# Performance work log

Measured on AMD Instinct MI355X. Metric: run time of the kernel, lower is better.

The kernel has to match this reference:

```python
import jax, jax.numpy as jnp
import numpy as np

TABLE = 4194304   # maxGridFeatId[-1]
D = 4             # eachGridFeatDim
L = 6             # gridFeatLevelCnt (code indexes sigma1..sigma6)
DIR = 16          # in_dim_dir
H = 64            # hidden_dim_color
B, N = 16384, 128


def _linear_init(key, fan_in, fan_out):
    # matches torch nn.Linear default U(-1/sqrt(fan_in), 1/sqrt(fan_in))
    s = 1.0 / np.sqrt(fan_in)
    kw, kb = jax.random.split(key)
    W = jax.random.uniform(kw, (fan_in, fan_out), minval=-s, maxval=s, dtype=jnp.float32)
    b = jax.random.uniform(kb, (fan_out,), minval=-s, maxval=s, dtype=jnp.float32)
    return W, b


def setup_inputs() -> dict:
    key = jax.random.key(0)
    ks = jax.random.split(key, 6)
    x = jax.random.randint(ks[0], (B, N, L), 0, TABLE)
    d = jax.random.normal(ks[1], (B, DIR), dtype=jnp.float32)
    gridWeight = jax.random.uniform(ks[2], (TABLE, D), dtype=jnp.float32)  # torch.rand
    in0 = DIR + L * (D - 1)  # 16 + 18 = 34
    W0, b0 = _linear_init(ks[3], in0, H)
    W1, b1 = _linear_init(ks[4], H, H)
    W2, b2 = _linear_init(ks[5], H, 3)
    return dict(x=x, d=d, gridWeight=gridWeight, W0=W0, b0=b0, W1=W1, b1=b1, W2=W2, b2=b2)


def reference(x, d, gridWeight, W0, b0, W1, b1, W2, b2):
    Bv, Nv, Lv = x.shape
    Dv = gridWeight.shape[-1]
    # embedding gather: (B, N, L, D); same memory order as torch reshape(B, N*L, D)
    feat = gridWeight[x]
    # per-level densities, clipped then multiplied (prod over the 6 levels)
    sig = jnp.clip(feat[..., 0], 0.0, 1.0)                 # (B, N, L)
    sigma0 = jnp.prod(sig, axis=-1, keepdims=True) + 1e-4  # (B, N, 1)
    sigma = sigma0 / jnp.max(sigma0, axis=1, keepdims=True)
    # geometric features: (B, N, L*(D-1))
    geo = feat[..., 1:].reshape(Bv, Nv, Lv * (Dv - 1))
    h = jnp.concatenate([jnp.broadcast_to(d[:, None, :], (Bv, Nv, d.shape[-1])), geo], axis=-1)
    h = jax.nn.relu(h @ W0 + b0)
    h = jax.nn.relu(h @ W1 + b1)
    color = jax.nn.sigmoid(h @ W2 + b2)                    # (B, N, 3)
    # alpha compositing: NOTE original does torch.cumprod(..., dim=2) on a
    # (B, N, 1) tensor, i.e. cumprod over a size-1 axis == identity. Faithful.
    alpha = 1.0 - sigma
    transparentBefore = jnp.concatenate(
        [jnp.ones((Bv, 1, 1), dtype=sigma.dtype), alpha[:, :-1]], axis=1)
    colorWeight0 = transparentBefore * sigma               # (B, N, 1)
    colorOut = colorWeight0 * color                        # (B, N, 3)
    return sigma, jnp.sum(colorOut, axis=1)                # (B,N,1), (B,3)
```

## Files before the change

### kernel.cpp

```cpp
#include <hip/hip_runtime.h>
#include <math.h>


typedef short bf16x8 __attribute__((ext_vector_type(8)));
typedef float floatx4 __attribute__((ext_vector_type(4)));

__device__ inline unsigned short f2b(float f) {
    union { float f; unsigned u; } v; v.f = f;
    unsigned r = v.u + 0x7FFF + ((v.u >> 16) & 1);
    return (unsigned short)(r >> 16);
}

__global__ void build_frags(const float* __restrict__ W0,
                            const float* __restrict__ W1,
                            const float* __restrict__ W2,
                            unsigned short* __restrict__ wsf) {
    int tid = blockIdx.x * blockDim.x + threadIdx.x;
    if (tid >= 7168) return;
    int lane, j, k, n;
    float val;
    if (tid < 2048) {
        int f = tid >> 9, r = tid & 511; lane = r >> 3; j = r & 7;
        k = ((lane >> 4) * 8) + j;
        n = f * 16 + (lane & 15);
        val = (k < 18) ? W0[(16 + k) * 64 + n] : 0.0f;
    } else if (tid < 6144) {
        int e = tid - 2048;
        int f = e >> 9, r = e & 511; lane = r >> 3; j = r & 7;
        int ks = f >> 2, nt = f & 3;
        k = ks * 32 + ((lane >> 4) * 8) + j;
        n = nt * 16 + (lane & 15);
        val = W1[k * 64 + n];
    } else {
        int e = tid - 6144;
        int f = e >> 9, r = e & 511; lane = r >> 3; j = r & 7;
        k = f * 32 + ((lane >> 4) * 8) + j;
        n = lane & 15;
        val = (n < 3) ? W2[k * 3 + n] : 0.0f;
    }
    wsf[tid] = f2b(val);
}

__global__ __launch_bounds__(512, 4) void surf_main(
    const int*   __restrict__ x,
    const float* __restrict__ dvec,
    const float* __restrict__ gw,
    const float* __restrict__ W0,
    const float* __restrict__ b0,
    const float* __restrict__ b1,
    const float* __restrict__ b2,
    const unsigned short* __restrict__ wsf,
    float* __restrict__ out_sigma,
    float* __restrict__ out_color)
{
    const int b    = blockIdx.x;
    const int t    = threadIdx.x;
    const int lane = t & 63;
    const int w    = t >> 6;
    const int l15  = lane & 15;
    const int quad = lane >> 4;

    __shared__ unsigned short A0[128 * 40];
    __shared__ unsigned short H1[128 * 72];
    __shared__ float s_sigl[768];
    __shared__ float s_dirW[64];
    __shared__ float s_wmax[2];
    __shared__ float s_cw[128];
    __shared__ float s_part[8 * 16];

    bf16x8 bw0[4], bw1[8];
    #pragma unroll
    for (int i = 0; i < 4; ++i) bw0[i] = *(const bf16x8*)(wsf + i * 512 + lane * 8);
    #pragma unroll
    for (int i = 0; i < 8; ++i) bw1[i] = *(const bf16x8*)(wsf + 2048 + i * 512 + lane * 8);

    #pragma unroll
    for (int e0 = 0; e0 < 768; e0 += 512) {
        int e = e0 + t;
        if (e < 768) {
            int xv = x[(size_t)b * 768 + e];
            int point = e / 6;
            int level = e - point * 6;
            float4 v = *(const float4*)(gw + (size_t)xv * 4);
            s_sigl[e] = fminf(fmaxf(v.x, 0.0f), 1.0f);
            unsigned short* a = A0 + point * 40 + level * 3;
            a[0] = f2b(v.y); a[1] = f2b(v.z); a[2] = f2b(v.w);
        }
    }
    if (t < 128) {
        unsigned short* a = A0 + t * 40;
        *(unsigned int*)(a + 18) = 0u;
        *(uint2*)(a + 20) = make_uint2(0u, 0u);
        *(uint2*)(a + 24) = make_uint2(0u, 0u);
        *(uint2*)(a + 28) = make_uint2(0u, 0u);
    }
    if (t < 64) {
        float acc = b0[t];
        const float* db = dvec + (size_t)b * 16;
        #pragma unroll
        for (int i = 0; i < 16; ++i) acc = fmaf(db[i], W0[i * 64 + t], acc);
        s_dirW[t] = acc;
    }
    __syncthreads();

    float sigma0 = 0.0f;
    if (t < 128) {
        float p = 1.0f;
        #pragma unroll
        for (int l = 0; l < 6; ++l) p *= s_sigl[t * 6 + l];
        sigma0 = p + 1e-4f;
        float m = sigma0;
        #pragma unroll
        for (int off = 32; off; off >>= 1) m = fmaxf(m, __shfl_xor(m, off));
        if (lane == 0) s_wmax[w] = m;
    }
    __syncthreads();
    if (t < 128) {
        float maxv  = fmaxf(s_wmax[0], s_wmax[1]);
        float sigma = sigma0 / maxv;
        out_sigma[(size_t)b * 128 + t] = sigma;
        float cw;
        if (t == 0) cw = sigma;
        else {
            float pp = 1.0f;
            #pragma unroll
            for (int l = 0; l < 6; ++l) pp *= s_sigl[(t - 1) * 6 + l];
            float sprev = (pp + 1e-4f) / maxv;
            cw = (1.0f - sprev) * sigma;
        }
        s_cw[t] = cw;
    }

    const int row = w * 16 + l15;
    bf16x8 a0 = *(const bf16x8*)(A0 + row * 40 + quad * 8);
    floatx4 acc0[4];
    #pragma unroll
    for (int nt = 0; nt < 4; ++nt) {
        float dw = s_dirW[nt * 16 + l15];
        acc0[nt] = (floatx4){dw, dw, dw, dw};
        acc0[nt] = __builtin_amdgcn_mfma_f32_16x16x32_bf16(a0, bw0[nt], acc0[nt], 0, 0, 0);
    }
    #pragma unroll
    for (int nt = 0; nt < 4; ++nt)
        #pragma unroll
        for (int r = 0; r < 4; ++r) {
            int pr = w * 16 + quad * 4 + r;
            H1[pr * 72 + nt * 16 + l15] = f2b(fmaxf(acc0[nt][r], 0.0f));
        }

    bf16x8 a1a = *(const bf16x8*)(H1 + row * 72 + quad * 8);
    bf16x8 a1b = *(const bf16x8*)(H1 + row * 72 + 32 + quad * 8);
    floatx4 acc1[4];
    #pragma unroll
    for (int nt = 0; nt < 4; ++nt) {
        float bb = b1[nt * 16 + l15];
        acc1[nt] = (floatx4){bb, bb, bb, bb};
        acc1[nt] = __builtin_amdgcn_mfma_f32_16x16x32_bf16(a1a, bw1[nt],     acc1[nt], 0, 0, 0);
        acc1[nt] = __builtin_amdgcn_mfma_f32_16x16x32_bf16(a1b, bw1[4 + nt], acc1[nt], 0, 0, 0);
    }
    #pragma unroll
    for (int nt = 0; nt < 4; ++nt)
        #pragma unroll
        for (int r = 0; r < 4; ++r) {
            int pr = w * 16 + quad * 4 + r;
            H1[pr * 72 + nt * 16 + l15] = f2b(fmaxf(acc1[nt][r], 0.0f));
        }

    bf16x8 bw2a = *(const bf16x8*)(wsf + 6144 + lane * 8);
    bf16x8 bw2b = *(const bf16x8*)(wsf + 6144 + 512 + lane * 8);
    bf16x8 a2a = *(const bf16x8*)(H1 + row * 72 + quad * 8);
    bf16x8 a2b = *(const bf16x8*)(H1 + row * 72 + 32 + quad * 8);
    float bias2 = (l15 < 3) ? b2[l15] : 0.0f;
    floatx4 acc2 = (floatx4){bias2, bias2, bias2, bias2};
    acc2 = __builtin_amdgcn_mfma_f32_16x16x32_bf16(a2a, bw2a, acc2, 0, 0, 0);
    acc2 = __builtin_amdgcn_mfma_f32_16x16x32_bf16(a2b, bw2b, acc2, 0, 0, 0);

    __syncthreads();
    float sum = 0.0f;
    #pragma unroll
    for (int r = 0; r < 4; ++r) {
        float col = 1.0f / (1.0f + __expf(-acc2[r]));
        float cw  = s_cw[w * 16 + quad * 4 + r];
        sum += cw * col;
    }
    sum += __shfl_xor(sum, 16);
    sum += __shfl_xor(sum, 32);
    if (lane < 16) s_part[w * 16 + lane] = sum;
    __syncthreads();
    if (t < 3) {
        float o = 0.0f;
        #pragma unroll
        for (int ww = 0; ww < 8; ++ww) o += s_part[ww * 16 + t];
        out_color[(size_t)b * 3 + t] = o;
    }
}

extern "C" void kernel_launch(void* const* d_in, const int* in_sizes, int n_in,
                              void* d_out, int out_size, void* d_ws, size_t ws_size,
                              hipStream_t stream) {
    const int*   x    = (const int*)d_in[0];
    const float* dvec = (const float*)d_in[1];
    const float* gw   = (const float*)d_in[2];
    const float* W0   = (const float*)d_in[3];
    const float* b0   = (const float*)d_in[4];
    const float* W1   = (const float*)d_in[5];
    const float* b1   = (const float*)d_in[6];
    const float* W2   = (const float*)d_in[7];
    const float* b2   = (const float*)d_in[8];

    const int B = in_sizes[1] / 16;
    float* out_sigma = (float*)d_out;
    float* out_color = (float*)d_out + (size_t)B * 128;
    unsigned short* wsf = (unsigned short*)d_ws;

    build_frags<<<14, 512, 0, stream>>>(W0, W1, W2, wsf);
    surf_main<<<B, 512, 0, stream>>>(x, dvec, gw, W0, b0, b1, b2, wsf,
                                     out_sigma, out_color);
}
```

Baseline: 338.3 us.

## Hoist gather loads, pack bf16 conversions, swizzle A0 layout, raise occupancy

Issues the x index and grid-feature gathers at kernel entry, before the weight-fragment loads, so the random global reads start earlier. Rewrites the A0 tile as a 32-column XOR-swizzled layout, with each level stored as a padded 4-element packed write, and remaps the W0 fragments to match. Replaces the software bf16 rounding with the hardware v_cvt_pk_bf16_f32 instruction and raises the launch-bounds occupancy hint from 4 to 8. The higher occupancy hint may force register spills, since each thread holds 12 weight fragments plus the early-loaded feature values.

```diff
diff --git a/kernel.cpp b/kernel.cpp
--- a/kernel.cpp
+++ b/kernel.cpp
@@ -4,11 +4,18 @@
 
 typedef short bf16x8 __attribute__((ext_vector_type(8)));
 typedef float floatx4 __attribute__((ext_vector_type(4)));
+typedef float f32x4  __attribute__((ext_vector_type(4)));
 
 __device__ inline unsigned short f2b(float f) {
     union { float f; unsigned u; } v; v.f = f;
     unsigned r = v.u + 0x7FFF + ((v.u >> 16) & 1);
     return (unsigned short)(r >> 16);
+}
+
+__device__ inline unsigned cvt_pk_bf16(float a, float b) {
+    unsigned r;
+    asm("v_cvt_pk_bf16_f32 %0, %1, %2" : "=v"(r) : "v"(a), "v"(b));
+    return r;
 }
 
 __global__ void build_frags(const float* __restrict__ W0,
@@ -21,9 +28,10 @@
     float val;
     if (tid < 2048) {
         int f = tid >> 9, r = tid & 511; lane = r >> 3; j = r & 7;
-        k = ((lane >> 4) * 8) + j;
+        int kp  = ((lane >> 4) * 8) + j;
+        int lev = kp >> 2, c = kp & 3;
         n = f * 16 + (lane & 15);
-        val = (k < 18) ? W0[(16 + k) * 64 + n] : 0.0f;
+        val = (lev < 6 && c < 3) ? W0[(16 + lev * 3 + c) * 64 + n] : 0.0f;
     } else if (tid < 6144) {
         int e = tid - 2048;
         int f = e >> 9, r = e & 511; lane = r >> 3; j = r & 7;
@@ -41,7 +49,7 @@
     wsf[tid] = f2b(val);
 }
 
-__global__ __launch_bounds__(512, 4) void surf_main(
+__global__ __launch_bounds__(512, 8) void surf_main(
     const int*   __restrict__ x,
     const float* __restrict__ dvec,
     const float* __restrict__ gw,
@@ -60,7 +68,7 @@
     const int l15  = lane & 15;
     const int quad = lane >> 4;
 
-    __shared__ unsigned short A0[128 * 40];
+    __shared__ __align__(16) unsigned short A0[128 * 32];
     __shared__ unsigned short H1[128 * 72];
     __shared__ float s_sigl[768];
     __shared__ float s_dirW[64];
@@ -68,31 +76,23 @@
     __shared__ float s_cw[128];
     __shared__ float s_part[8 * 16];
 
+    const size_t b768 = (size_t)b * 768;
+
+    int xv1 = x[b768 + t];
+    int xv2 = (w < 4) ? x[b768 + 512 + t] : 0;
+    f32x4 v1 = *(const f32x4*)(gw + (size_t)xv1 * 4);
+    f32x4 v2 = {};
+    if (w < 4) v2 = *(const f32x4*)(gw + (size_t)xv2 * 4);
+
     bf16x8 bw0[4], bw1[8];
     #pragma unroll
     for (int i = 0; i < 4; ++i) bw0[i] = *(const bf16x8*)(wsf + i * 512 + lane * 8);
     #pragma unroll
     for (int i = 0; i < 8; ++i) bw1[i] = *(const bf16x8*)(wsf + 2048 + i * 512 + lane * 8);
 
-    #pragma unroll
-    for (int e0 = 0; e0 < 768; e0 += 512) {
-        int e = e0 + t;
-        if (e < 768) {
-            int xv = x[(size_t)b * 768 + e];
-            int point = e / 6;
-            int level = e - point * 6;
-            float4 v = *(const float4*)(gw + (size_t)xv * 4);
-            s_sigl[e] = fminf(fmaxf(v.x, 0.0f), 1.0f);
-            unsigned short* a = A0 + point * 40 + level * 3;
-            a[0] = f2b(v.y); a[1] = f2b(v.z); a[2] = f2b(v.w);
-        }
-    }
     if (t < 128) {
-        unsigned short* a = A0 + t * 40;
-        *(unsigned int*)(a + 18) = 0u;
-        *(uint2*)(a + 20) = make_uint2(0u, 0u);
-        *(uint2*)(a + 24) = make_uint2(0u, 0u);
-        *(uint2*)(a + 28) = make_uint2(0u, 0u);
+        int p = t;
+        *(uint4*)(A0 + p * 32 + ((3 ^ (p & 3)) << 3)) = make_uint4(0u, 0u, 0u, 0u);
     }
     if (t < 64) {
         float acc = b0[t];
@@ -100,6 +100,23 @@
         #pragma unroll
         for (int i = 0; i < 16; ++i) acc = fmaf(db[i], W0[i * 64 + t], acc);
         s_dirW[t] = acc;
+    }
+
+    {
+        int e = t, p = e / 6, l = e - p * 6;
+        s_sigl[e] = fminf(fmaxf(v1.x, 0.0f), 1.0f);
+        uint2 pk;
+        pk.x = cvt_pk_bf16(v1.y, v1.z);
+        pk.y = cvt_pk_bf16(v1.w, 0.0f);
+        *(uint2*)(A0 + p * 32 + (((l >> 1) ^ (p & 3)) << 3) + ((l & 1) << 2)) = pk;
+    }
+    if (w < 4) {
+        int e = 512 + t, p = e / 6, l = e - p * 6;
+        s_sigl[e] = fminf(fmaxf(v2.x, 0.0f), 1.0f);
+        uint2 pk;
+        pk.x = cvt_pk_bf16(v2.y, v2.z);
+        pk.y = cvt_pk_bf16(v2.w, 0.0f);
+        *(uint2*)(A0 + p * 32 + (((l >> 1) ^ (p & 3)) << 3) + ((l & 1) << 2)) = pk;
     }
     __syncthreads();
 
@@ -132,7 +149,8 @@
     }
 
     const int row = w * 16 + l15;
-    bf16x8 a0 = *(const bf16x8*)(A0 + row * 40 + quad * 8);
+    const int swz = l15 & 3;
+    bf16x8 a0 = *(const bf16x8*)(A0 + row * 32 + ((quad ^ swz) << 3));
     floatx4 acc0[4];
     #pragma unroll
     for (int nt = 0; nt < 4; ++nt) {
@@ -145,7 +163,8 @@
         #pragma unroll
         for (int r = 0; r < 4; ++r) {
             int pr = w * 16 + quad * 4 + r;
-            H1[pr * 72 + nt * 16 + l15] = f2b(fmaxf(acc0[nt][r], 0.0f));
+            H1[pr * 72 + nt * 16 + l15] =
+                (unsigned short)cvt_pk_bf16(fmaxf(acc0[nt][r], 0.0f), 0.0f);
         }
 
     bf16x8 a1a = *(const bf16x8*)(H1 + row * 72 + quad * 8);
@@ -163,7 +182,8 @@
         #pragma unroll
         for (int r = 0; r < 4; ++r) {
             int pr = w * 16 + quad * 4 + r;
-            H1[pr * 72 + nt * 16 + l15] = f2b(fmaxf(acc1[nt][r], 0.0f));
+            H1[pr * 72 + nt * 16 + l15] =
+                (unsigned short)cvt_pk_bf16(fmaxf(acc1[nt][r], 0.0f), 0.0f);
         }
 
     bf16x8 bw2a = *(const bf16x8*)(wsf + 6144 + lane * 8);
```

Result: slower. 457.6 us (+35.2%).
